# Optimization experiments

Measured on AMD Instinct MI355X. Metric: run time of the kernel, lower is better.

The kernel has to match this reference:

```python
import jax, jax.numpy as jnp
import numpy as np

N = 100000          # nodes
E = 1600000         # edges (avg degree 16)
D = 128             # prototype feature dim
C = 100             # num classes
NUM_LAYERS = 3      # propagation layers


def setup_inputs() -> dict:
    key = jax.random.key(0)
    k1, k2, k3, k4 = jax.random.split(key, 4)
    train_mask = jax.random.randint(k1, (N,), 0, 2) > 0                # bool [N]
    labels_all = jax.random.randint(k2, (N,), 0, C)                    # int   [N]
    edge_index = jax.random.randint(k3, (2, E), 0, N)                  # int   [2,E]
    global_protos = jax.random.normal(k4, (C, D), dtype=jnp.float32)   # [C,D]
    alpha = jnp.float32(0.5)                                           # learnable scalar
    return dict(train_mask=train_mask, global_protos=global_protos,
                labels_all=labels_all, edge_index=edge_index, alpha=alpha)


def _label_propagate(y0, edge_index, alpha):
    # symmetric GCN normalization D^-1/2 A D^-1/2 (no self loops), as in PyG LabelPropagation
    src, dst = edge_index[0], edge_index[1]
    deg = jax.ops.segment_sum(jnp.ones((E,), y0.dtype), dst, num_segments=N)
    deg_inv_sqrt = jnp.where(deg > 0, jax.lax.rsqrt(jnp.maximum(deg, 1.0)), 0.0)
    norm = deg_inv_sqrt[src] * deg_inv_sqrt[dst]                       # [E]
    res = (1.0 - alpha) * y0                                           # residual term
    out = y0
    for _ in range(NUM_LAYERS):
        msgs = out[src] * norm[:, None]                                # gather [E,D]
        agg = jax.ops.segment_sum(msgs, dst, num_segments=N)           # scatter-add [N,D]
        out = jnp.clip(alpha * agg + res, 0.0, 1.0)                    # post_step clamp
    return out


def reference(train_mask, global_protos, labels_all, edge_index, alpha):
    # proto_rep[train_mask] = global_protos[labels_all[train_mask]], zeros elsewhere
    y0 = jnp.where(train_mask[:, None], global_protos[labels_all], 0.0)  # [N,D]
    return _label_propagate(y0, edge_index, alpha)
```

## Files before the change

kernel.cpp:

```cpp
#include <hip/hip_runtime.h>
#include <stdint.h>

#define N_NODES 100000
#define N_EDGES 1600000
#define CAP     64
#define NC      196
#define SLOTS   40
#define SEGCAP  12288
#define EPB     4096


__global__ __launch_bounds__(256) void bin_kernel(
    const int* __restrict__ src, const int* __restrict__ dst,
    int* __restrict__ gcur, unsigned int* __restrict__ gbins) {
    __shared__ int lcnt[NC];
    __shared__ int gb[NC];
    __shared__ unsigned int lbuf[NC * SLOTS];
    int t = threadIdx.x;
    for (int b = t; b < NC; b += 256) lcnt[b] = 0;
    __syncthreads();

    int base = blockIdx.x * EPB;
    int sv[16], dv[16];
#pragma unroll
    for (int k = 0; k < 16; ++k) {
        int i = base + k * 256 + t;
        sv[k] = (i < N_EDGES) ? src[i] : -1;
        dv[k] = (i < N_EDGES) ? dst[i] : 0;
    }
#pragma unroll
    for (int k = 0; k < 16; ++k) {
        if (sv[k] >= 0) {
            int d = dv[k];
            int cb = d >> 9;
            unsigned rec = (unsigned)sv[k] | ((unsigned)(d & 511) << 17);
            int pos = atomicAdd(&lcnt[cb], 1);
            if (pos < SLOTS) {
                lbuf[cb * SLOTS + pos] = rec;
            } else {
                int gp = atomicAdd(&gcur[cb], 1);
                if (gp < SEGCAP) gbins[(size_t)cb * SEGCAP + gp] = rec;
            }
        }
    }
    __syncthreads();
    if (t < NC) {
        int c = lcnt[t]; if (c > SLOTS) c = SLOTS;
        gb[t] = atomicAdd(&gcur[t], c);
    }
    __syncthreads();
    int wave = t >> 6, lane = t & 63;
    for (int b = wave; b < NC; b += 4) {
        int c = lcnt[b]; if (c > SLOTS) c = SLOTS;
        if (lane < c)
            gbins[(size_t)b * SEGCAP + gb[b] + lane] = lbuf[b * SLOTS + lane];
    }
}


__global__ __launch_bounds__(512) void csr_kernel(
    const unsigned int* __restrict__ gbins, const int* __restrict__ gcur,
    int* __restrict__ cnt, int* __restrict__ csr, float* __restrict__ dis,
    const int* __restrict__ mask, const int* __restrict__ labels,
    int* __restrict__ c0) {
    __shared__ int lc[512];
    int b = blockIdx.x;
    int t = threadIdx.x;
    lc[t] = 0;
    __syncthreads();
    int m = gcur[b]; if (m > SEGCAP) m = SEGCAP;
    const unsigned int* seg = gbins + (size_t)b * SEGCAP;
    int base = b << 9;
    for (int i = t; i < m; i += 512) {
        unsigned int v = seg[i];
        int dl = (int)(v >> 17);
        int pos = atomicAdd(&lc[dl], 1);
        if (pos < CAP) csr[(size_t)(base + dl) * CAP + pos] = (int)(v & 0x1FFFF);
    }
    __syncthreads();
    int n = base + t;
    if (n < N_NODES) {
        int d = lc[t];
        cnt[n] = d;
        dis[n] = (d > 0) ? rsqrtf((float)d) : 0.0f;
        c0[n] = mask[n] ? labels[n] : -1;
    }
}

template <int MODE>
__global__ __launch_bounds__(256) void prop_kernel(
    const uchar4* __restrict__ cur, void* __restrict__ out,
    const int* __restrict__ cnt, const int* __restrict__ csr,
    const float* __restrict__ dis, const int* __restrict__ c0,
    const float* __restrict__ protos, const float* __restrict__ alpha_p) {
    int wave = threadIdx.x >> 6;
    int lane = threadIdx.x & 63;
    int half = lane >> 5;
    int sub  = lane & 31;
    int base_lane = half << 5;
    int n = blockIdx.x * 8 + wave * 2 + half;

    float alpha = *alpha_p;
    int m = cnt[n];
    if (m > CAP) m = CAP;
    float dn = dis[n];
    const int* bucket = csr + (size_t)n * CAP;
    const float4* proto4 = (const float4*)protos;
    const float inv255 = 1.0f / 255.0f;

    int sl = 0;  float wl = 0.f;  int cl = -1;
    if (sub < m) {
        sl = bucket[sub];
        wl = dis[sl] * dn;
        if (MODE == 0) cl = c0[sl];
    }
    int sl2 = 0; float wl2 = 0.f; int cl2 = -1;
    if (m > 32 && 32 + sub < m) {
        sl2 = bucket[32 + sub];
        wl2 = dis[sl2] * dn;
        if (MODE == 0) cl2 = c0[sl2];
    }
    int m_other = __shfl(m, lane ^ 32);
    int mmax = m > m_other ? m : m_other;

    float a0 = 0.f, a1 = 0.f, a2 = 0.f, a3 = 0.f;

    if (MODE == 0) {
        for (int j = 0; j < mmax; j += 4) {
            float w[4]; float4 v[4];
            bool lo = j < 32;
#pragma unroll
            for (int k = 0; k < 4; ++k) {
                int e = j + k;
                float ww; int c;
                if (lo) { ww = __shfl(wl,  base_lane + e);      c = __shfl(cl,  base_lane + e); }
                else    { ww = __shfl(wl2, base_lane + e - 32); c = __shfl(cl2, base_lane + e - 32); }
                w[k] = ww;
                v[k] = (c >= 0) ? proto4[c * 32 + sub] : make_float4(0.f, 0.f, 0.f, 0.f);
            }
#pragma unroll
            for (int k = 0; k < 4; ++k) {
                a0 = fmaf(w[k], v[k].x, a0);
                a1 = fmaf(w[k], v[k].y, a1);
                a2 = fmaf(w[k], v[k].z, a2);
                a3 = fmaf(w[k], v[k].w, a3);
            }
        }
    } else {
        uchar4 u[8];  float w[8];
        uchar4 u2[8]; float w2[8];
#pragma unroll
        for (int k = 0; k < 8; ++k) {
            float ww = __shfl(wl, base_lane + k);
            int   s  = __shfl(sl, base_lane + k);
            w[k] = ww;
            u[k] = cur[(size_t)s * 32 + sub];
        }
        for (int j = 0; j < mmax; j += 8) {
            int jn = j + 8;
            if (jn < mmax) {
                bool lo = jn < 32;
#pragma unroll
                for (int k = 0; k < 8; ++k) {
                    int e = jn + k;
                    float ww; int s;
                    if (lo) { ww = __shfl(wl,  base_lane + e);      s = __shfl(sl,  base_lane + e); }
                    else    { ww = __shfl(wl2, base_lane + e - 32); s = __shfl(sl2, base_lane + e - 32); }
                    w2[k] = ww;
                    u2[k] = cur[(size_t)s * 32 + sub];
                }
            }
#pragma unroll
            for (int k = 0; k < 8; ++k) {
                float ws = w[k] * inv255;
                a0 = fmaf(ws, (float)u[k].x, a0);
                a1 = fmaf(ws, (float)u[k].y, a1);
                a2 = fmaf(ws, (float)u[k].z, a2);
                a3 = fmaf(ws, (float)u[k].w, a3);
            }
#pragma unroll
            for (int k = 0; k < 8; ++k) { u[k] = u2[k]; w[k] = w2[k]; }
        }
    }

    float y0x = 0.f, y0y = 0.f, y0z = 0.f, y0w = 0.f;
    int cn = c0[n];
    if (cn >= 0) {
        float4 p = proto4[cn * 32 + sub];
        y0x = p.x; y0y = p.y; y0z = p.z; y0w = p.w;
    }
    float ra = 1.f - alpha;
    float o0 = fminf(fmaxf(fmaf(alpha, a0, ra * y0x), 0.f), 1.f);
    float o1 = fminf(fmaxf(fmaf(alpha, a1, ra * y0y), 0.f), 1.f);
    float o2 = fminf(fmaxf(fmaf(alpha, a2, ra * y0z), 0.f), 1.f);
    float o3 = fminf(fmaxf(fmaf(alpha, a3, ra * y0w), 0.f), 1.f);

    if (MODE == 2) {
        ((float4*)out)[(size_t)n * 32 + sub] = make_float4(o0, o1, o2, o3);
    } else {
        uchar4 q;
        q.x = (unsigned char)(o0 * 255.f + 0.5f);
        q.y = (unsigned char)(o1 * 255.f + 0.5f);
        q.z = (unsigned char)(o2 * 255.f + 0.5f);
        q.w = (unsigned char)(o3 * 255.f + 0.5f);
        ((uchar4*)out)[(size_t)n * 32 + sub] = q;
    }
}


extern "C" void kernel_launch(void* const* d_in, const int* in_sizes, int n_in,
                              void* d_out, int out_size, void* d_ws, size_t ws_size,
                              hipStream_t stream) {
    const int*   mask   = (const int*)d_in[0];
    const float* protos = (const float*)d_in[1];
    const int*   labels = (const int*)d_in[2];
    const int*   ei     = (const int*)d_in[3];
    const float* alpha  = (const float*)d_in[4];
    const int* src = ei;
    const int* dst = ei + N_EDGES;

    int*          gcur  = (int*)d_ws;
    int*          cnt   = gcur + 256;
    float*        dis   = (float*)(cnt + N_NODES);
    int*          c0    = (int*)(dis + N_NODES);
    int*          csr   = c0 + N_NODES;
    unsigned int* gbins = (unsigned int*)(csr + (size_t)N_NODES * CAP);
    uchar4*       bufA  = (uchar4*)(gbins + (size_t)NC * SEGCAP);
    uchar4*       bufB  = bufA + (size_t)N_NODES * 32;

    hipMemsetAsync(gcur, 0, 256 * sizeof(int), stream);

    int bgrid = (N_EDGES + EPB - 1) / EPB;
    bin_kernel<<<bgrid, 256, 0, stream>>>(src, dst, gcur, gbins);
    csr_kernel<<<NC, 512, 0, stream>>>(gbins, gcur, cnt, csr, dis,
                                       mask, labels, c0);

    int pgrid = N_NODES / 8;
    prop_kernel<0><<<pgrid, 256, 0, stream>>>(nullptr, bufA, cnt, csr, dis, c0,
                                              protos, alpha);
    prop_kernel<1><<<pgrid, 256, 0, stream>>>(bufA, bufB, cnt, csr, dis, c0,
                                              protos, alpha);
    prop_kernel<2><<<pgrid, 256, 0, stream>>>(bufB, d_out, cnt, csr, dis, c0,
                                              protos, alpha);
}
```

Before: 226.6 us.

## Split CSR build blocks in half and stage prototypes in LDS for layer 0

The CSR build kernel now launches two blocks per destination bin. Each block scans the whole segment but keeps only the 256 destinations in its half, which doubles parallelism across the 196 bins at the cost of reading every segment twice. Layer 0 moves into a dedicated kernel with 1024 threads that loads the 100x128 prototype table into shared memory (51 KB) and gathers from there instead of global memory. The large LDS allocation and block size may limit occupancy.

```diff
diff --git a/kernel.cpp b/kernel.cpp
--- a/kernel.cpp
+++ b/kernel.cpp
@@ -63,28 +63,118 @@
     int* __restrict__ cnt, int* __restrict__ csr, float* __restrict__ dis,
     const int* __restrict__ mask, const int* __restrict__ labels,
     int* __restrict__ c0) {
-    __shared__ int lc[512];
-    int b = blockIdx.x;
+    __shared__ int lc[256];
+    int b    = blockIdx.x >> 1;
+    int half = blockIdx.x & 1;
     int t = threadIdx.x;
-    lc[t] = 0;
+    if (t < 256) lc[t] = 0;
     __syncthreads();
     int m = gcur[b]; if (m > SEGCAP) m = SEGCAP;
     const unsigned int* seg = gbins + (size_t)b * SEGCAP;
-    int base = b << 9;
+    int base = (b << 9) + (half << 8);
     for (int i = t; i < m; i += 512) {
         unsigned int v = seg[i];
         int dl = (int)(v >> 17);
-        int pos = atomicAdd(&lc[dl], 1);
-        if (pos < CAP) csr[(size_t)(base + dl) * CAP + pos] = (int)(v & 0x1FFFF);
-    }
-    __syncthreads();
-    int n = base + t;
-    if (n < N_NODES) {
-        int d = lc[t];
-        cnt[n] = d;
-        dis[n] = (d > 0) ? rsqrtf((float)d) : 0.0f;
-        c0[n] = mask[n] ? labels[n] : -1;
-    }
+        if ((dl >> 8) == half) {
+            int local = dl & 255;
+            int pos = atomicAdd(&lc[local], 1);
+            if (pos < CAP) csr[(size_t)(base + local) * CAP + pos] = (int)(v & 0x1FFFF);
+        }
+    }
+    __syncthreads();
+    if (t < 256) {
+        int n = base + t;
+        if (n < N_NODES) {
+            int d = lc[t];
+            cnt[n] = d;
+            dis[n] = (d > 0) ? rsqrtf((float)d) : 0.0f;
+            c0[n] = mask[n] ? labels[n] : -1;
+        }
+    }
+}
+
+
+
+__global__ __launch_bounds__(1024) void prop0_kernel(
+    uchar4* __restrict__ out,
+    const int* __restrict__ cnt, const int* __restrict__ csr,
+    const float* __restrict__ dis, const int* __restrict__ c0,
+    const float* __restrict__ protos, const float* __restrict__ alpha_p) {
+    __shared__ float4 sp[100 * 32];
+    int t = threadIdx.x;
+    const float4* proto4 = (const float4*)protos;
+    for (int i = t; i < 100 * 32; i += 1024) sp[i] = proto4[i];
+    __syncthreads();
+
+    int wave = t >> 6;
+    int lane = t & 63;
+    int half = lane >> 5;
+    int sub  = lane & 31;
+    int base_lane = half << 5;
+    int n = blockIdx.x * 32 + wave * 2 + half;
+
+    float alpha = *alpha_p;
+    int m = cnt[n];
+    if (m > CAP) m = CAP;
+    float dn = dis[n];
+    const int* bucket = csr + (size_t)n * CAP;
+
+    int sl = 0;  float wl = 0.f;  int cl = -1;
+    if (sub < m) {
+        sl = bucket[sub];
+        wl = dis[sl] * dn;
+        cl = c0[sl];
+    }
+    float wl2 = 0.f; int cl2 = -1;
+    if (m > 32 && 32 + sub < m) {
+        int s2 = bucket[32 + sub];
+        wl2 = dis[s2] * dn;
+        cl2 = c0[s2];
+    }
+    int m_other = __shfl(m, lane ^ 32);
+    int mmax = m > m_other ? m : m_other;
+
+    float a0 = 0.f, a1 = 0.f, a2 = 0.f, a3 = 0.f;
+
+    for (int j = 0; j < mmax; j += 4) {
+        float w[4]; float4 v[4];
+        bool lo = j < 32;
+#pragma unroll
+        for (int k = 0; k < 4; ++k) {
+            int e = j + k;
+            float ww; int c;
+            if (lo) { ww = __shfl(wl,  base_lane + e);      c = __shfl(cl,  base_lane + e); }
+            else    { ww = __shfl(wl2, base_lane + e - 32); c = __shfl(cl2, base_lane + e - 32); }
+            w[k] = ww;
+            v[k] = (c >= 0) ? sp[c * 32 + sub] : make_float4(0.f, 0.f, 0.f, 0.f);
+        }
+#pragma unroll
+        for (int k = 0; k < 4; ++k) {
+            a0 = fmaf(w[k], v[k].x, a0);
+            a1 = fmaf(w[k], v[k].y, a1);
+            a2 = fmaf(w[k], v[k].z, a2);
+            a3 = fmaf(w[k], v[k].w, a3);
+        }
+    }
+
+    float y0x = 0.f, y0y = 0.f, y0z = 0.f, y0w = 0.f;
+    int cn = c0[n];
+    if (cn >= 0) {
+        float4 p = sp[cn * 32 + sub];
+        y0x = p.x; y0y = p.y; y0z = p.z; y0w = p.w;
+    }
+    float ra = 1.f - alpha;
+    float o0 = fminf(fmaxf(fmaf(alpha, a0, ra * y0x), 0.f), 1.f);
+    float o1 = fminf(fmaxf(fmaf(alpha, a1, ra * y0y), 0.f), 1.f);
+    float o2 = fminf(fmaxf(fmaf(alpha, a2, ra * y0z), 0.f), 1.f);
+    float o3 = fminf(fmaxf(fmaf(alpha, a3, ra * y0w), 0.f), 1.f);
+
+    uchar4 q;
+    q.x = (unsigned char)(o0 * 255.f + 0.5f);
+    q.y = (unsigned char)(o1 * 255.f + 0.5f);
+    q.z = (unsigned char)(o2 * 255.f + 0.5f);
+    q.w = (unsigned char)(o3 * 255.f + 0.5f);
+    out[(size_t)n * 32 + sub] = q;
 }
 
 template <int MODE>
@@ -108,79 +198,54 @@
     const float4* proto4 = (const float4*)protos;
     const float inv255 = 1.0f / 255.0f;
 
-    int sl = 0;  float wl = 0.f;  int cl = -1;
+    int sl = 0;  float wl = 0.f;
     if (sub < m) {
         sl = bucket[sub];
         wl = dis[sl] * dn;
-        if (MODE == 0) cl = c0[sl];
-    }
-    int sl2 = 0; float wl2 = 0.f; int cl2 = -1;
+    }
+    int sl2 = 0; float wl2 = 0.f;
     if (m > 32 && 32 + sub < m) {
         sl2 = bucket[32 + sub];
         wl2 = dis[sl2] * dn;
-        if (MODE == 0) cl2 = c0[sl2];
     }
     int m_other = __shfl(m, lane ^ 32);
     int mmax = m > m_other ? m : m_other;
 
     float a0 = 0.f, a1 = 0.f, a2 = 0.f, a3 = 0.f;
 
-    if (MODE == 0) {
-        for (int j = 0; j < mmax; j += 4) {
-            float w[4]; float4 v[4];
-            bool lo = j < 32;
-#pragma unroll
-            for (int k = 0; k < 4; ++k) {
-                int e = j + k;
-                float ww; int c;
-                if (lo) { ww = __shfl(wl,  base_lane + e);      c = __shfl(cl,  base_lane + e); }
-                else    { ww = __shfl(wl2, base_lane + e - 32); c = __shfl(cl2, base_lane + e - 32); }
-                w[k] = ww;
-                v[k] = (c >= 0) ? proto4[c * 32 + sub] : make_float4(0.f, 0.f, 0.f, 0.f);
+    uchar4 u[8];  float w[8];
+    uchar4 u2[8]; float w2[8];
+#pragma unroll
+    for (int k = 0; k < 8; ++k) {
+        float ww = __shfl(wl, base_lane + k);
+        int   s  = __shfl(sl, base_lane + k);
+        w[k] = ww;
+        u[k] = cur[(size_t)s * 32 + sub];
+    }
+    for (int j = 0; j < mmax; j += 8) {
+        int jn = j + 8;
+        if (jn < mmax) {
+            bool lo = jn < 32;
+#pragma unroll
+            for (int k = 0; k < 8; ++k) {
+                int e = jn + k;
+                float ww; int s;
+                if (lo) { ww = __shfl(wl,  base_lane + e);      s = __shfl(sl,  base_lane + e); }
+                else    { ww = __shfl(wl2, base_lane + e - 32); s = __shfl(sl2, base_lane + e - 32); }
+                w2[k] = ww;
+                u2[k] = cur[(size_t)s * 32 + sub];
             }
-#pragma unroll
-            for (int k = 0; k < 4; ++k) {
-                a0 = fmaf(w[k], v[k].x, a0);
-                a1 = fmaf(w[k], v[k].y, a1);
-                a2 = fmaf(w[k], v[k].z, a2);
-                a3 = fmaf(w[k], v[k].w, a3);
-            }
-        }
-    } else {
-        uchar4 u[8];  float w[8];
-        uchar4 u2[8]; float w2[8];
+        }
 #pragma unroll
         for (int k = 0; k < 8; ++k) {
-            float ww = __shfl(wl, base_lane + k);
-            int   s  = __shfl(sl, base_lane + k);
-            w[k] = ww;
-            u[k] = cur[(size_t)s * 32 + sub];
-        }
-        for (int j = 0; j < mmax; j += 8) {
-            int jn = j + 8;
-            if (jn < mmax) {
-                bool lo = jn < 32;
-#pragma unroll
-                for (int k = 0; k < 8; ++k) {
-                    int e = jn + k;
-                    float ww; int s;
-                    if (lo) { ww = __shfl(wl,  base_lane + e);      s = __shfl(sl,  base_lane + e); }
-                    else    { ww = __shfl(wl2, base_lane + e - 32); s = __shfl(sl2, base_lane + e - 32); }
-                    w2[k] = ww;
-                    u2[k] = cur[(size_t)s * 32 + sub];
-                }
-            }
-#pragma unroll
-            for (int k = 0; k < 8; ++k) {
-                float ws = w[k] * inv255;
-                a0 = fmaf(ws, (float)u[k].x, a0);
-                a1 = fmaf(ws, (float)u[k].y, a1);
-                a2 = fmaf(ws, (float)u[k].z, a2);
-                a3 = fmaf(ws, (float)u[k].w, a3);
-            }
-#pragma unroll
-            for (int k = 0; k < 8; ++k) { u[k] = u2[k]; w[k] = w2[k]; }
-        }
+            float ws = w[k] * inv255;
+            a0 = fmaf(ws, (float)u[k].x, a0);
+            a1 = fmaf(ws, (float)u[k].y, a1);
+            a2 = fmaf(ws, (float)u[k].z, a2);
+            a3 = fmaf(ws, (float)u[k].w, a3);
+        }
+#pragma unroll
+        for (int k = 0; k < 8; ++k) { u[k] = u2[k]; w[k] = w2[k]; }
     }
 
     float y0x = 0.f, y0y = 0.f, y0z = 0.f, y0w = 0.f;
@@ -232,12 +297,12 @@
 
     int bgrid = (N_EDGES + EPB - 1) / EPB;
     bin_kernel<<<bgrid, 256, 0, stream>>>(src, dst, gcur, gbins);
-    csr_kernel<<<NC, 512, 0, stream>>>(gbins, gcur, cnt, csr, dis,
-                                       mask, labels, c0);
-
+    csr_kernel<<<NC * 2, 512, 0, stream>>>(gbins, gcur, cnt, csr, dis,
+                                           mask, labels, c0);
+
+    prop0_kernel<<<N_NODES / 32, 1024, 0, stream>>>(bufA, cnt, csr, dis, c0,
+                                                    protos, alpha);
     int pgrid = N_NODES / 8;
-    prop_kernel<0><<<pgrid, 256, 0, stream>>>(nullptr, bufA, cnt, csr, dis, c0,
-                                              protos, alpha);
     prop_kernel<1><<<pgrid, 256, 0, stream>>>(bufA, bufB, cnt, csr, dis, c0,
                                               protos, alpha);
     prop_kernel<2><<<pgrid, 256, 0, stream>>>(bufB, d_out, cnt, csr, dis, c0,
```

New measurement: 233.3 us. +3.0%, slower.

## Assign one wave per node and stage edge metadata in shared memory

Applied to the files above, without the earlier changes.

The propagation kernel now gives each node a full 64-lane wave, with each lane owning two features, instead of two nodes per wave at four features per lane. Neighbor weights and source indices are staged once per wave in shared memory and read back as float4 broadcasts, replacing per-edge cross-lane shuffles. The loop is padded to multiples of eight with zero-weight entries, and the missing-label branch is dropped by folding it into the weight. Gather width per lane shrinks to 2-byte and 8-byte loads, which may cut memory efficiency per request, and the grid doubles in block count.

```diff
diff --git a/kernel.cpp b/kernel.cpp
--- a/kernel.cpp
+++ b/kernel.cpp
@@ -87,123 +87,134 @@
     }
 }
 
+
 template <int MODE>
 __global__ __launch_bounds__(256) void prop_kernel(
-    const uchar4* __restrict__ cur, void* __restrict__ out,
+    const uint8_t* __restrict__ cur, void* __restrict__ out,
     const int* __restrict__ cnt, const int* __restrict__ csr,
     const float* __restrict__ dis, const int* __restrict__ c0,
     const float* __restrict__ protos, const float* __restrict__ alpha_p) {
+    __shared__ float2 smeta[4][CAP];
     int wave = threadIdx.x >> 6;
     int lane = threadIdx.x & 63;
-    int half = lane >> 5;
-    int sub  = lane & 31;
-    int base_lane = half << 5;
-    int n = blockIdx.x * 8 + wave * 2 + half;
+    int n = blockIdx.x * 4 + wave;
 
     float alpha = *alpha_p;
     int m = cnt[n];
     if (m > CAP) m = CAP;
     float dn = dis[n];
     const int* bucket = csr + (size_t)n * CAP;
-    const float4* proto4 = (const float4*)protos;
     const float inv255 = 1.0f / 255.0f;
 
-    int sl = 0;  float wl = 0.f;  int cl = -1;
-    if (sub < m) {
-        sl = bucket[sub];
-        wl = dis[sl] * dn;
-        if (MODE == 0) cl = c0[sl];
-    }
-    int sl2 = 0; float wl2 = 0.f; int cl2 = -1;
-    if (m > 32 && 32 + sub < m) {
-        sl2 = bucket[32 + sub];
-        wl2 = dis[sl2] * dn;
-        if (MODE == 0) cl2 = c0[sl2];
-    }
-    int m_other = __shfl(m, lane ^ 32);
-    int mmax = m > m_other ? m : m_other;
-
-    float a0 = 0.f, a1 = 0.f, a2 = 0.f, a3 = 0.f;
+    float w = 0.f; int sc = 0;
+    if (lane < m) {
+        int s = bucket[lane];
+        w = dis[s] * dn;
+        if (MODE == 0) {
+            int c = c0[s];
+            if (c < 0) { w = 0.f; sc = 0; } else sc = c;
+        } else {
+            sc = s;
+            w *= inv255;
+        }
+    }
+    smeta[wave][lane] = make_float2(w, __int_as_float(sc));
+    __syncthreads();
+
+    const float4* sm4 = (const float4*)&smeta[wave][0];
+    int mp = (m + 7) & ~7;
+
+    float a0 = 0.f, a1 = 0.f;
 
     if (MODE == 0) {
-        for (int j = 0; j < mmax; j += 4) {
-            float w[4]; float4 v[4];
-            bool lo = j < 32;
+        float wA[8]; int sA[8]; float2 vA[8];
+        float wB[8]; int sB[8]; float2 vB[8];
+        if (mp > 0) {
 #pragma unroll
             for (int k = 0; k < 4; ++k) {
-                int e = j + k;
-                float ww; int c;
-                if (lo) { ww = __shfl(wl,  base_lane + e);      c = __shfl(cl,  base_lane + e); }
-                else    { ww = __shfl(wl2, base_lane + e - 32); c = __shfl(cl2, base_lane + e - 32); }
-                w[k] = ww;
-                v[k] = (c >= 0) ? proto4[c * 32 + sub] : make_float4(0.f, 0.f, 0.f, 0.f);
-            }
+                float4 q = sm4[k];
+                wA[2*k]   = q.x; sA[2*k]   = __float_as_int(q.y);
+                wA[2*k+1] = q.z; sA[2*k+1] = __float_as_int(q.w);
+            }
+#pragma unroll
+            for (int k = 0; k < 8; ++k)
+                vA[k] = *(const float2*)(protos + (size_t)sA[k] * 128 + lane * 2);
+        }
+        for (int j = 0; j < mp; j += 8) {
+            int jn = j + 8;
+            if (jn < mp) {
+#pragma unroll
+                for (int k = 0; k < 4; ++k) {
+                    float4 q = sm4[(jn >> 1) + k];
+                    wB[2*k]   = q.x; sB[2*k]   = __float_as_int(q.y);
+                    wB[2*k+1] = q.z; sB[2*k+1] = __float_as_int(q.w);
+                }
+#pragma unroll
+                for (int k = 0; k < 8; ++k)
+                    vB[k] = *(const float2*)(protos + (size_t)sB[k] * 128 + lane * 2);
+            }
+#pragma unroll
+            for (int k = 0; k < 8; ++k) {
+                a0 = fmaf(wA[k], vA[k].x, a0);
+                a1 = fmaf(wA[k], vA[k].y, a1);
+            }
+#pragma unroll
+            for (int k = 0; k < 8; ++k) { wA[k] = wB[k]; vA[k] = vB[k]; }
+        }
+    } else {
+        float wA[8]; int sA[8]; unsigned uA[8];
+        float wB[8]; int sB[8]; unsigned uB[8];
+        if (mp > 0) {
 #pragma unroll
             for (int k = 0; k < 4; ++k) {
-                a0 = fmaf(w[k], v[k].x, a0);
-                a1 = fmaf(w[k], v[k].y, a1);
-                a2 = fmaf(w[k], v[k].z, a2);
-                a3 = fmaf(w[k], v[k].w, a3);
-            }
-        }
-    } else {
-        uchar4 u[8];  float w[8];
-        uchar4 u2[8]; float w2[8];
-#pragma unroll
-        for (int k = 0; k < 8; ++k) {
-            float ww = __shfl(wl, base_lane + k);
-            int   s  = __shfl(sl, base_lane + k);
-            w[k] = ww;
-            u[k] = cur[(size_t)s * 32 + sub];
-        }
-        for (int j = 0; j < mmax; j += 8) {
+                float4 q = sm4[k];
+                wA[2*k]   = q.x; sA[2*k]   = __float_as_int(q.y);
+                wA[2*k+1] = q.z; sA[2*k+1] = __float_as_int(q.w);
+            }
+#pragma unroll
+            for (int k = 0; k < 8; ++k)
+                uA[k] = *(const unsigned short*)(cur + (size_t)sA[k] * 128 + lane * 2);
+        }
+        for (int j = 0; j < mp; j += 8) {
             int jn = j + 8;
-            if (jn < mmax) {
-                bool lo = jn < 32;
-#pragma unroll
-                for (int k = 0; k < 8; ++k) {
-                    int e = jn + k;
-                    float ww; int s;
-                    if (lo) { ww = __shfl(wl,  base_lane + e);      s = __shfl(sl,  base_lane + e); }
-                    else    { ww = __shfl(wl2, base_lane + e - 32); s = __shfl(sl2, base_lane + e - 32); }
-                    w2[k] = ww;
-                    u2[k] = cur[(size_t)s * 32 + sub];
+            if (jn < mp) {
+#pragma unroll
+                for (int k = 0; k < 4; ++k) {
+                    float4 q = sm4[(jn >> 1) + k];
+                    wB[2*k]   = q.x; sB[2*k]   = __float_as_int(q.y);
+                    wB[2*k+1] = q.z; sB[2*k+1] = __float_as_int(q.w);
                 }
+#pragma unroll
+                for (int k = 0; k < 8; ++k)
+                    uB[k] = *(const unsigned short*)(cur + (size_t)sB[k] * 128 + lane * 2);
             }
 #pragma unroll
             for (int k = 0; k < 8; ++k) {
-                float ws = w[k] * inv255;
-                a0 = fmaf(ws, (float)u[k].x, a0);
-                a1 = fmaf(ws, (float)u[k].y, a1);
-                a2 = fmaf(ws, (float)u[k].z, a2);
-                a3 = fmaf(ws, (float)u[k].w, a3);
-            }
-#pragma unroll
-            for (int k = 0; k < 8; ++k) { u[k] = u2[k]; w[k] = w2[k]; }
-        }
-    }
-
-    float y0x = 0.f, y0y = 0.f, y0z = 0.f, y0w = 0.f;
+                a0 = fmaf(wA[k], (float)(uA[k] & 0xffu), a0);
+                a1 = fmaf(wA[k], (float)(uA[k] >> 8),   a1);
+            }
+#pragma unroll
+            for (int k = 0; k < 8; ++k) { wA[k] = wB[k]; uA[k] = uB[k]; }
+        }
+    }
+
+    float y00 = 0.f, y01 = 0.f;
     int cn = c0[n];
     if (cn >= 0) {
-        float4 p = proto4[cn * 32 + sub];
-        y0x = p.x; y0y = p.y; y0z = p.z; y0w = p.w;
+        float2 p = *(const float2*)(protos + (size_t)cn * 128 + lane * 2);
+        y00 = p.x; y01 = p.y;
     }
     float ra = 1.f - alpha;
-    float o0 = fminf(fmaxf(fmaf(alpha, a0, ra * y0x), 0.f), 1.f);
-    float o1 = fminf(fmaxf(fmaf(alpha, a1, ra * y0y), 0.f), 1.f);
-    float o2 = fminf(fmaxf(fmaf(alpha, a2, ra * y0z), 0.f), 1.f);
-    float o3 = fminf(fmaxf(fmaf(alpha, a3, ra * y0w), 0.f), 1.f);
+    float o0 = fminf(fmaxf(fmaf(alpha, a0, ra * y00), 0.f), 1.f);
+    float o1 = fminf(fmaxf(fmaf(alpha, a1, ra * y01), 0.f), 1.f);
 
     if (MODE == 2) {
-        ((float4*)out)[(size_t)n * 32 + sub] = make_float4(o0, o1, o2, o3);
+        ((float2*)out)[(size_t)n * 64 + lane] = make_float2(o0, o1);
     } else {
-        uchar4 q;
-        q.x = (unsigned char)(o0 * 255.f + 0.5f);
-        q.y = (unsigned char)(o1 * 255.f + 0.5f);
-        q.z = (unsigned char)(o2 * 255.f + 0.5f);
-        q.w = (unsigned char)(o3 * 255.f + 0.5f);
-        ((uchar4*)out)[(size_t)n * 32 + sub] = q;
+        unsigned q0 = (unsigned)(o0 * 255.f + 0.5f);
+        unsigned q1 = (unsigned)(o1 * 255.f + 0.5f);
+        ((unsigned short*)out)[(size_t)n * 64 + lane] =
+            (unsigned short)(q0 | (q1 << 8));
     }
 }
 
@@ -225,8 +236,8 @@
     int*          c0    = (int*)(dis + N_NODES);
     int*          csr   = c0 + N_NODES;
     unsigned int* gbins = (unsigned int*)(csr + (size_t)N_NODES * CAP);
-    uchar4*       bufA  = (uchar4*)(gbins + (size_t)NC * SEGCAP);
-    uchar4*       bufB  = bufA + (size_t)N_NODES * 32;
+    uint8_t*      bufA  = (uint8_t*)(gbins + (size_t)NC * SEGCAP);
+    uint8_t*      bufB  = bufA + (size_t)N_NODES * 128;
 
     hipMemsetAsync(gcur, 0, 256 * sizeof(int), stream);
 
@@ -235,7 +246,7 @@
     csr_kernel<<<NC, 512, 0, stream>>>(gbins, gcur, cnt, csr, dis,
                                        mask, labels, c0);
 
-    int pgrid = N_NODES / 8;
+    int pgrid = N_NODES / 4;
     prop_kernel<0><<<pgrid, 256, 0, stream>>>(nullptr, bufA, cnt, csr, dis, c0,
                                               protos, alpha);
     prop_kernel<1><<<pgrid, 256, 0, stream>>>(bufA, bufB, cnt, csr, dis, c0,
```

Measured after the change: 295.5 us. 30.4% more time.

## Switch intermediates to fp16 rows with 16-lane groups and LDS edge metadata

Applied to the files above, without the earlier changes.

Intermediate layer buffers now hold fp16 instead of 8-bit quantized values, and the prototypes are converted to fp16 so layer 0 uses the same gather path. Each node is handled by a 16-lane group loading 16-byte rows. Edge weights and row offsets are staged in shared memory and the gathers are double-buffered, replacing the per-edge shuffles. The intent is wider, fewer memory transactions and less shuffle overhead, at the cost of twice the intermediate gather bytes compared with 8-bit and reuse of the bin scratch region for buffers.

```diff
diff --git a/kernel.cpp b/kernel.cpp
--- a/kernel.cpp
+++ b/kernel.cpp
@@ -1,5 +1,7 @@
 #include <hip/hip_runtime.h>
 #include <stdint.h>
+
+typedef _Float16 f16;
 
 #define N_NODES 100000
 #define N_EDGES 1600000
@@ -62,7 +64,8 @@
     const unsigned int* __restrict__ gbins, const int* __restrict__ gcur,
     int* __restrict__ cnt, int* __restrict__ csr, float* __restrict__ dis,
     const int* __restrict__ mask, const int* __restrict__ labels,
-    int* __restrict__ c0) {
+    int* __restrict__ c0, const float* __restrict__ protos,
+    f16* __restrict__ pf16) {
     __shared__ int lc[512];
     int b = blockIdx.x;
     int t = threadIdx.x;
@@ -85,125 +88,108 @@
         dis[n] = (d > 0) ? rsqrtf((float)d) : 0.0f;
         c0[n] = mask[n] ? labels[n] : -1;
     }
-}
+    if (b < 25) pf16[b * 512 + t] = (f16)protos[b * 512 + t];
+}
+
 
 template <int MODE>
 __global__ __launch_bounds__(256) void prop_kernel(
-    const uchar4* __restrict__ cur, void* __restrict__ out,
+    const f16* __restrict__ rows, void* __restrict__ out,
     const int* __restrict__ cnt, const int* __restrict__ csr,
     const float* __restrict__ dis, const int* __restrict__ c0,
     const float* __restrict__ protos, const float* __restrict__ alpha_p) {
-    int wave = threadIdx.x >> 6;
-    int lane = threadIdx.x & 63;
-    int half = lane >> 5;
-    int sub  = lane & 31;
-    int base_lane = half << 5;
-    int n = blockIdx.x * 8 + wave * 2 + half;
+    __shared__ uint2 smeta[4][4][CAP];
+    int t = threadIdx.x;
+    int wave = t >> 6, lane = t & 63;
+    int grp = lane >> 4, s16 = lane & 15;
+    int n = blockIdx.x * 16 + wave * 4 + grp;
 
     float alpha = *alpha_p;
-    int m = cnt[n];
-    if (m > CAP) m = CAP;
+    int m = cnt[n]; if (m > CAP) m = CAP;
     float dn = dis[n];
     const int* bucket = csr + (size_t)n * CAP;
-    const float4* proto4 = (const float4*)protos;
-    const float inv255 = 1.0f / 255.0f;
-
-    int sl = 0;  float wl = 0.f;  int cl = -1;
-    if (sub < m) {
-        sl = bucket[sub];
-        wl = dis[sl] * dn;
-        if (MODE == 0) cl = c0[sl];
-    }
-    int sl2 = 0; float wl2 = 0.f; int cl2 = -1;
-    if (m > 32 && 32 + sub < m) {
-        sl2 = bucket[32 + sub];
-        wl2 = dis[sl2] * dn;
-        if (MODE == 0) cl2 = c0[sl2];
-    }
-    int m_other = __shfl(m, lane ^ 32);
-    int mmax = m > m_other ? m : m_other;
-
-    float a0 = 0.f, a1 = 0.f, a2 = 0.f, a3 = 0.f;
-
-    if (MODE == 0) {
-        for (int j = 0; j < mmax; j += 4) {
-            float w[4]; float4 v[4];
-            bool lo = j < 32;
-#pragma unroll
-            for (int k = 0; k < 4; ++k) {
-                int e = j + k;
-                float ww; int c;
-                if (lo) { ww = __shfl(wl,  base_lane + e);      c = __shfl(cl,  base_lane + e); }
-                else    { ww = __shfl(wl2, base_lane + e - 32); c = __shfl(cl2, base_lane + e - 32); }
-                w[k] = ww;
-                v[k] = (c >= 0) ? proto4[c * 32 + sub] : make_float4(0.f, 0.f, 0.f, 0.f);
+
+    int mm = m;
+    { int o = __shfl_xor(mm, 16); mm = mm > o ? mm : o;
+      o = __shfl_xor(mm, 32);     mm = mm > o ? mm : o; }
+    int mp = (mm + 3) & ~3;
+
+    for (int e = s16; e < mp; e += 16) {
+        unsigned wb = 0, off = 0;
+        if (e < m) {
+            int s = bucket[e];
+            float w = dis[s] * dn;
+            if (MODE == 0) {
+                int c = c0[s];
+                if (c < 0) w = 0.f; else off = (unsigned)c << 4;
+            } else {
+                off = (unsigned)s << 4;
             }
-#pragma unroll
-            for (int k = 0; k < 4; ++k) {
-                a0 = fmaf(w[k], v[k].x, a0);
-                a1 = fmaf(w[k], v[k].y, a1);
-                a2 = fmaf(w[k], v[k].z, a2);
-                a3 = fmaf(w[k], v[k].w, a3);
-            }
+            wb = __float_as_uint(w);
         }
+        smeta[wave][grp][e] = make_uint2(wb, off);
+    }
+
+    const uint4* md = (const uint4*)&smeta[wave][grp][0];
+    const uint4* r4 = (const uint4*)rows;
+
+    float acc[8] = {0.f, 0.f, 0.f, 0.f, 0.f, 0.f, 0.f, 0.f};
+
+    uint4 mA0, mA1, gA0, gA1, gA2, gA3;
+    uint4 mB0, mB1, gB0, gB1, gB2, gB3;
+
+#define LOADB(MM0, MM1, G0, G1, G2, G3, J) do {            \
+    MM0 = md[(J) >> 1]; MM1 = md[((J) >> 1) + 1];          \
+    G0 = r4[MM0.y + s16]; G1 = r4[MM0.w + s16];            \
+    G2 = r4[MM1.y + s16]; G3 = r4[MM1.w + s16]; } while (0)
+
+#define COMP1(WB, G) do {                                  \
+    union { uint4 u; f16 h[8]; } q_; q_.u = (G);           \
+    float w_ = __uint_as_float(WB);                        \
+    _Pragma("unroll")                                      \
+    for (int i_ = 0; i_ < 8; ++i_)                         \
+        acc[i_] = fmaf((float)q_.h[i_], w_, acc[i_]); } while (0)
+
+#define COMP(MM0, MM1, G0, G1, G2, G3) do {                \
+    COMP1(MM0.x, G0); COMP1(MM0.z, G1);                    \
+    COMP1(MM1.x, G2); COMP1(MM1.z, G3); } while (0)
+
+    if (mp > 0) {
+        LOADB(mA0, mA1, gA0, gA1, gA2, gA3, 0);
+        for (int j = 0; j < mp; j += 8) {
+            if (j + 4 < mp) LOADB(mB0, mB1, gB0, gB1, gB2, gB3, j + 4);
+            COMP(mA0, mA1, gA0, gA1, gA2, gA3);
+            if (j + 8 < mp) LOADB(mA0, mA1, gA0, gA1, gA2, gA3, j + 8);
+            if (j + 4 < mp) COMP(mB0, mB1, gB0, gB1, gB2, gB3);
+        }
+    }
+#undef LOADB
+#undef COMP1
+#undef COMP
+
+    int cn = c0[n];
+    float ra = 1.f - alpha;
+    float y[8] = {0.f, 0.f, 0.f, 0.f, 0.f, 0.f, 0.f, 0.f};
+    if (cn >= 0) {
+        const float4* pr = (const float4*)(protos + (size_t)cn * 128) + (s16 << 1);
+        float4 p0 = pr[0], p1 = pr[1];
+        y[0] = p0.x; y[1] = p0.y; y[2] = p0.z; y[3] = p0.w;
+        y[4] = p1.x; y[5] = p1.y; y[6] = p1.z; y[7] = p1.w;
+    }
+    float o[8];
+#pragma unroll
+    for (int i = 0; i < 8; ++i)
+        o[i] = fminf(fmaxf(fmaf(alpha, acc[i], ra * y[i]), 0.f), 1.f);
+
+    if (MODE == 2) {
+        float4* dst = (float4*)out + ((size_t)n << 5) + (s16 << 1);
+        dst[0] = make_float4(o[0], o[1], o[2], o[3]);
+        dst[1] = make_float4(o[4], o[5], o[6], o[7]);
     } else {
-        uchar4 u[8];  float w[8];
-        uchar4 u2[8]; float w2[8];
-#pragma unroll
-        for (int k = 0; k < 8; ++k) {
-            float ww = __shfl(wl, base_lane + k);
-            int   s  = __shfl(sl, base_lane + k);
-            w[k] = ww;
-            u[k] = cur[(size_t)s * 32 + sub];
-        }
-        for (int j = 0; j < mmax; j += 8) {
-            int jn = j + 8;
-            if (jn < mmax) {
-                bool lo = jn < 32;
-#pragma unroll
-                for (int k = 0; k < 8; ++k) {
-                    int e = jn + k;
-                    float ww; int s;
-                    if (lo) { ww = __shfl(wl,  base_lane + e);      s = __shfl(sl,  base_lane + e); }
-                    else    { ww = __shfl(wl2, base_lane + e - 32); s = __shfl(sl2, base_lane + e - 32); }
-                    w2[k] = ww;
-                    u2[k] = cur[(size_t)s * 32 + sub];
-                }
-            }
-#pragma unroll
-            for (int k = 0; k < 8; ++k) {
-                float ws = w[k] * inv255;
-                a0 = fmaf(ws, (float)u[k].x, a0);
-                a1 = fmaf(ws, (float)u[k].y, a1);
-                a2 = fmaf(ws, (float)u[k].z, a2);
-                a3 = fmaf(ws, (float)u[k].w, a3);
-            }
-#pragma unroll
-            for (int k = 0; k < 8; ++k) { u[k] = u2[k]; w[k] = w2[k]; }
-        }
-    }
-
-    float y0x = 0.f, y0y = 0.f, y0z = 0.f, y0w = 0.f;
-    int cn = c0[n];
-    if (cn >= 0) {
-        float4 p = proto4[cn * 32 + sub];
-        y0x = p.x; y0y = p.y; y0z = p.z; y0w = p.w;
-    }
-    float ra = 1.f - alpha;
-    float o0 = fminf(fmaxf(fmaf(alpha, a0, ra * y0x), 0.f), 1.f);
-    float o1 = fminf(fmaxf(fmaf(alpha, a1, ra * y0y), 0.f), 1.f);
-    float o2 = fminf(fmaxf(fmaf(alpha, a2, ra * y0z), 0.f), 1.f);
-    float o3 = fminf(fmaxf(fmaf(alpha, a3, ra * y0w), 0.f), 1.f);
-
-    if (MODE == 2) {
-        ((float4*)out)[(size_t)n * 32 + sub] = make_float4(o0, o1, o2, o3);
-    } else {
-        uchar4 q;
-        q.x = (unsigned char)(o0 * 255.f + 0.5f);
-        q.y = (unsigned char)(o1 * 255.f + 0.5f);
-        q.z = (unsigned char)(o2 * 255.f + 0.5f);
-        q.w = (unsigned char)(o3 * 255.f + 0.5f);
-        ((uchar4*)out)[(size_t)n * 32 + sub] = q;
+        union { uint4 u; f16 h[8]; } q;
+#pragma unroll
+        for (int i = 0; i < 8; ++i) q.h[i] = (f16)o[i];
+        ((uint4*)out)[((size_t)n << 4) + s16] = q.u;
     }
 }
 
@@ -224,19 +210,21 @@
     float*        dis   = (float*)(cnt + N_NODES);
     int*          c0    = (int*)(dis + N_NODES);
     int*          csr   = c0 + N_NODES;
-    unsigned int* gbins = (unsigned int*)(csr + (size_t)N_NODES * CAP);
-    uchar4*       bufA  = (uchar4*)(gbins + (size_t)NC * SEGCAP);
-    uchar4*       bufB  = bufA + (size_t)N_NODES * 32;
+    f16*          pf16  = (f16*)(csr + (size_t)N_NODES * CAP);
+    unsigned char* region = (unsigned char*)(pf16 + 16384);
+    unsigned int* gbins = (unsigned int*)region;
+    f16*          bufA  = (f16*)region;
+    f16*          bufB  = bufA + (size_t)N_NODES * 128;
 
     hipMemsetAsync(gcur, 0, 256 * sizeof(int), stream);
 
     int bgrid = (N_EDGES + EPB - 1) / EPB;
     bin_kernel<<<bgrid, 256, 0, stream>>>(src, dst, gcur, gbins);
     csr_kernel<<<NC, 512, 0, stream>>>(gbins, gcur, cnt, csr, dis,
-                                       mask, labels, c0);
-
-    int pgrid = N_NODES / 8;
-    prop_kernel<0><<<pgrid, 256, 0, stream>>>(nullptr, bufA, cnt, csr, dis, c0,
+                                       mask, labels, c0, protos, pf16);
+
+    int pgrid = N_NODES / 16;
+    prop_kernel<0><<<pgrid, 256, 0, stream>>>(pf16, bufA, cnt, csr, dis, c0,
                                               protos, alpha);
     prop_kernel<1><<<pgrid, 256, 0, stream>>>(bufA, bufB, cnt, csr, dis, c0,
                                               protos, alpha);
```

Result: slower. 274.7 us (+21.2%).
